# Kernel optimization log

Measured on AMD Instinct MI355X. Metric: run time of the kernel, lower is better.

The kernel has to match this reference:

```python
import jax, jax.numpy as jnp
import numpy as np

ALPHA = 1.0
B, N = 4096, 512


def _tv1d_row(y, lam):
    """Condat's direct 1-D TV denoising (exact port of the C reference used by prox_tv1d)."""
    n = y.shape[0]
    dt = y.dtype
    lam = jnp.asarray(lam, dt)
    idx = jnp.arange(n)

    def cond(s):
        return ~s[9]

    def body(s):
        k, k0, km, kp, vmin, vmax, umin, umax, x, done = s
        at_end = k == n - 1
        ynext = y[jnp.minimum(k + 1, n - 1)]
        # negative / positive jump tests (end-phase uses umin/umax sign tests)
        neg = jnp.where(at_end, umin < 0.0, ynext + umin < vmin - lam)
        pos = (~neg) & jnp.where(at_end, umax > 0.0, ynext + umax > vmax + lam)
        mid = (~neg) & (~pos)
        fin = mid & at_end
        mneg = neg & (~at_end)
        mpos = pos & (~at_end)
        mmid = mid & (~at_end)
        eneg = neg & at_end
        epos = pos & at_end
        # flush a finished segment of the output
        cnt_fin = (k - k0 + 1).astype(dt)
        hi = jnp.where(neg, km, jnp.where(pos, kp, n - 1))
        val = jnp.where(pos, vmax, jnp.where(fin, vmin + umin / cnt_fin, vmin))
        do_w = neg | pos | fin
        x = jnp.where(do_w & (idx >= k0) & (idx <= hi), val, x)
        nk = jnp.where(neg, km + 1, jnp.where(pos, kp + 1, k + 1))
        nk = jnp.minimum(nk, n - 1)
        ynk = y[nk]
        # plain accumulation step
        umin_t = umin + ynk - vmin
        umax_t = umax + ynk - vmax
        cnt = (nk - k0 + 1).astype(dt)
        c1 = umin_t >= lam
        c2 = umax_t <= -lam
        vmin_mid = jnp.where(c1, vmin + (umin_t - lam) / cnt, vmin)
        umin_mid = jnp.where(c1, lam, umin_t)
        km_mid = jnp.where(c1, nk, km)
        vmax_mid = jnp.where(c2, vmax + (umax_t + lam) / cnt, vmax)
        umax_mid = jnp.where(c2, -lam, umax_t)
        kp_mid = jnp.where(c2, nk, kp)
        jump = neg | pos
        nk0 = jnp.where(jump, nk, k0)
        nkm = jnp.where(neg | mpos, nk, jnp.where(mmid, km_mid, km))
        nkp = jnp.where(pos | mneg, nk, jnp.where(mmid, kp_mid, kp))
        nvmin = jnp.where(neg, ynk, jnp.where(mpos, ynk - 2.0 * lam, jnp.where(mmid, vmin_mid, vmin)))
        nvmax = jnp.where(pos, ynk, jnp.where(mneg, ynk + 2.0 * lam, jnp.where(mmid, vmax_mid, vmax)))
        numin = jnp.where(neg | mpos, lam, jnp.where(epos, ynk - lam - vmin, jnp.where(mmid, umin_mid, umin)))
        numax = jnp.where(pos | mneg, -lam, jnp.where(eneg, ynk + lam - vmax, jnp.where(mmid, umax_mid, umax)))
        nkk = jnp.where(fin, k, nk)
        return (nkk, nk0, nkm, nkp, nvmin, nvmax, numin, numax, x, done | fin)

    z = jnp.int32(0)
    s0 = (z, z, z, z, y[0] - lam, y[0] + lam, lam, -lam, jnp.zeros_like(y), jnp.array(False))
    return jax.lax.while_loop(cond, body, s0)[8]


def tv_prox(x, lam):
    return jax.vmap(lambda r: _tv1d_row(r, lam))(x)


def sparsemax(z):
    n = z.shape[-1]
    zs = -jnp.sort(-z, axis=-1)          # descending sort
    zc = jnp.cumsum(zs, axis=-1)
    r = jnp.arange(1, n + 1, dtype=z.dtype)
    supp = zs * r > (zc - 1.0)
    k = jnp.sum(supp, axis=-1, keepdims=True)
    tau = (jnp.take_along_axis(zc, k - 1, axis=-1) - 1.0) / k.astype(z.dtype)
    d = z - tau
    return jnp.where(d > 0.0, d, 0.0)


def setup_inputs():
    key = jax.random.key(0)
    x = jax.random.normal(key, (B, N), dtype=jnp.float32)
    return {"x": x}


def reference(x):
    # fusedmax(x) = sparsemax(prox_TV(x, alpha)), row-wise
    return sparsemax(tv_prox(x, ALPHA))
```

## Files before the change

kernel.cpp:

```cpp
#include <hip/hip_runtime.h>


#define TVN 512
#define LAMBDA 1.0f

__device__ __forceinline__ float wave_reduce_sum(float v) {
#pragma unroll
    for (int off = 32; off > 0; off >>= 1) v += __shfl_xor(v, off, 64);
    return v;
}

__global__ __launch_bounds__(64) void fusedmax_kernel(const float* __restrict__ xin,
                                                      float* __restrict__ out) {
    __shared__ alignas(16) float row[TVN + 8];
    const int t = threadIdx.x;
    const long long r = blockIdx.x;
    const float lam = LAMBDA;

    const float4* __restrict__ g4 = (const float4*)(xin + r * TVN);
    float4* s4 = (float4*)row;
    s4[t] = g4[t];
    s4[t + 64] = g4[t + 64];
    if (t < 8) row[TVN + t] = 0.0f;
    __syncthreads();

    if (t == 0) {
        const float yLast = row[TVN - 1];
        const float twolam = 2.0f * lam;
        int k = 0, k0 = 0, km = 0, kp = 0;
        float vmin = row[0] - lam, vmax = row[0] + lam;
        float umin = lam, umax = -lam;
        float cntf = 1.0f;
        float yn;

#define ACCUM_STEP(W)                                                   \
        yn = (W);                                                       \
        if (yn + umin < vmin - lam) goto neg_jump;                      \
        if (yn + umax > vmax + lam) goto pos_jump;                      \
        ++k; cntf += 1.0f;                                              \
        umin += yn - vmin;                                              \
        umax += yn - vmax;                                              \
        if (umin >= lam) {                                              \
            vmin += (umin - lam) * __builtin_amdgcn_rcpf(cntf);         \
            umin = lam; km = k;                                         \
        }                                                               \
        if (umax <= -lam) {                                             \
            vmax += (umax + lam) * __builtin_amdgcn_rcpf(cntf);         \
            umax = -lam; kp = k;                                        \
        }                                                               \
        if (k == TVN - 1) goto end_phase;

    refill: {
            float w0 = row[k + 1], w1 = row[k + 2], w2 = row[k + 3], w3 = row[k + 4];
            float w4 = row[k + 5], w5 = row[k + 6], w6 = row[k + 7], w7 = row[k + 8];
            ACCUM_STEP(w0)
            ACCUM_STEP(w1)
            ACCUM_STEP(w2)
            ACCUM_STEP(w3)
            ACCUM_STEP(w4)
            ACCUM_STEP(w5)
            ACCUM_STEP(w6)
            ACCUM_STEP(w7)
            goto refill;
        }
#undef ACCUM_STEP

    neg_jump: {
            for (int i = k0; i <= km; ++i) row[i] = vmin;
            const int nk = km + 1;
            const float ynk = row[nk];
            k = k0 = km = kp = nk;
            vmin = ynk;
            vmax = ynk + twolam;
            umin = lam;
            umax = -lam;
            cntf = 1.0f;
            if (k == TVN - 1) goto end_phase;
            goto refill;
        }

    pos_jump: {
            for (int i = k0; i <= kp; ++i) row[i] = vmax;
            const int nk = kp + 1;
            const float ynk = row[nk];
            k = k0 = km = kp = nk;
            vmax = ynk;
            vmin = ynk - twolam;
            umin = lam;
            umax = -lam;
            cntf = 1.0f;
            if (k == TVN - 1) goto end_phase;
            goto refill;
        }

    end_phase: {
            if (umin < 0.0f) {
                for (int i = k0; i <= km; ++i) row[i] = vmin;
                int nk = km + 1;
                const float ynk = (nk > TVN - 1) ? yLast : row[nk];
                if (nk > TVN - 1) nk = TVN - 1;
                k = k0 = km = nk;
                vmin = ynk;
                umin = lam;
                umax = ynk + lam - vmax;
                cntf = 1.0f;
                if (k == TVN - 1) goto end_phase;
                goto refill;
            } else if (umax > 0.0f) {
                for (int i = k0; i <= kp; ++i) row[i] = vmax;
                int nk = kp + 1;
                const float ynk = (nk > TVN - 1) ? yLast : row[nk];
                if (nk > TVN - 1) nk = TVN - 1;
                k = k0 = kp = nk;
                vmax = ynk;
                umax = -lam;
                umin = ynk - lam - vmin;
                cntf = 1.0f;
                if (k == TVN - 1) goto end_phase;
                goto refill;
            } else {
                const float v = vmin + umin / (float)(k - k0 + 1);
                for (int i = k0; i < TVN; ++i) row[i] = v;
            }
        }
    }
    __syncthreads();

    float4 a = s4[t];
    float4 b = s4[t + 64];
    float v[8] = {a.x, a.y, a.z, a.w, b.x, b.y, b.z, b.w};

    float ls = v[0] + v[1] + v[2] + v[3] + v[4] + v[5] + v[6] + v[7];
    float S = wave_reduce_sum(ls);
    float tau = (S - 1.0f) * (1.0f / (float)TVN);
    int cprev = TVN;
#pragma unroll 1
    for (int it = 0; it < 64; ++it) {
        float s = 0.0f, c = 0.0f;
#pragma unroll
        for (int j = 0; j < 8; ++j) {
            if (v[j] > tau) { s += v[j]; c += 1.0f; }
        }
        s = wave_reduce_sum(s);
        c = wave_reduce_sum(c);
        tau = (s - 1.0f) / c;
        int ci = (int)c;
        if (ci == cprev) break;
        cprev = ci;
    }

    float4 oa, ob;
    oa.x = fmaxf(v[0] - tau, 0.0f);
    oa.y = fmaxf(v[1] - tau, 0.0f);
    oa.z = fmaxf(v[2] - tau, 0.0f);
    oa.w = fmaxf(v[3] - tau, 0.0f);
    ob.x = fmaxf(v[4] - tau, 0.0f);
    ob.y = fmaxf(v[5] - tau, 0.0f);
    ob.z = fmaxf(v[6] - tau, 0.0f);
    ob.w = fmaxf(v[7] - tau, 0.0f);
    float4* __restrict__ o4 = (float4*)(out + r * TVN);
    o4[t] = oa;
    o4[t + 64] = ob;
}

extern "C" void kernel_launch(void* const* d_in, const int* in_sizes, int n_in,
                              void* d_out, int out_size, void* d_ws, size_t ws_size,
                              hipStream_t stream) {
    const float* x = (const float*)d_in[0];
    float* out = (float*)d_out;
    const int rows = in_sizes[0] / TVN;
    fusedmax_kernel<<<dim3(rows), dim3(64), 0, stream>>>(x, out);
}
```

Before: 262.5 us.

## Run TV denoising scan from both ends in parallel waves

Splits the serial Condat TV scan across two waves. One wave scans the row forward and the other scans a reversed copy, and each stops once a finalized segment reaches past the midpoint. The two halves are then stitched together for the sparsemax step, which roughly halves the serial dependency chain per row. The cost is a second shared buffer, a reversed staging copy, and redundant work when a segment straddles the midpoint. Correctness depends on finalized segments being exact in both scan directions.

```diff
diff --git a/kernel.cpp b/kernel.cpp
--- a/kernel.cpp
+++ b/kernel.cpp
@@ -3,6 +3,7 @@
 
 #define TVN 512
 #define LAMBDA 1.0f
+#define STOPK 257
 
 __device__ __forceinline__ float wave_reduce_sum(float v) {
 #pragma unroll
@@ -10,125 +11,153 @@
     return v;
 }
 
-__global__ __launch_bounds__(64) void fusedmax_kernel(const float* __restrict__ xin,
-                                                      float* __restrict__ out) {
-    __shared__ alignas(16) float row[TVN + 8];
-    const int t = threadIdx.x;
-    const long long r = blockIdx.x;
+__device__ __forceinline__ void tv_scan_half(float* __restrict__ row) {
     const float lam = LAMBDA;
-
-    const float4* __restrict__ g4 = (const float4*)(xin + r * TVN);
-    float4* s4 = (float4*)row;
-    s4[t] = g4[t];
-    s4[t + 64] = g4[t + 64];
-    if (t < 8) row[TVN + t] = 0.0f;
-    __syncthreads();
-
-    if (t == 0) {
-        const float yLast = row[TVN - 1];
-        const float twolam = 2.0f * lam;
-        int k = 0, k0 = 0, km = 0, kp = 0;
-        float vmin = row[0] - lam, vmax = row[0] + lam;
-        float umin = lam, umax = -lam;
-        float cntf = 1.0f;
-        float yn;
+    const float yLast = row[TVN - 1];
+    const float twolam = 2.0f * lam;
+    int k = 0, k0 = 0, km = 0, kp = 0;
+    float vmin = row[0] - lam, vmax = row[0] + lam;
+    float umin = lam, umax = -lam;
+    float cntf = 1.0f;
+    float yn;
 
 #define ACCUM_STEP(W)                                                   \
-        yn = (W);                                                       \
-        if (yn + umin < vmin - lam) goto neg_jump;                      \
-        if (yn + umax > vmax + lam) goto pos_jump;                      \
-        ++k; cntf += 1.0f;                                              \
-        umin += yn - vmin;                                              \
-        umax += yn - vmax;                                              \
-        if (umin >= lam) {                                              \
-            vmin += (umin - lam) * __builtin_amdgcn_rcpf(cntf);         \
-            umin = lam; km = k;                                         \
-        }                                                               \
-        if (umax <= -lam) {                                             \
-            vmax += (umax + lam) * __builtin_amdgcn_rcpf(cntf);         \
-            umax = -lam; kp = k;                                        \
-        }                                                               \
+    yn = (W);                                                           \
+    if (yn + umin < vmin - lam) goto neg_jump;                          \
+    if (yn + umax > vmax + lam) goto pos_jump;                          \
+    ++k; cntf += 1.0f;                                                  \
+    umin += yn - vmin;                                                  \
+    umax += yn - vmax;                                                  \
+    if (umin >= lam) {                                                  \
+        vmin += (umin - lam) * __builtin_amdgcn_rcpf(cntf);             \
+        umin = lam; km = k;                                             \
+    }                                                                   \
+    if (umax <= -lam) {                                                 \
+        vmax += (umax + lam) * __builtin_amdgcn_rcpf(cntf);             \
+        umax = -lam; kp = k;                                            \
+    }                                                                   \
+    if (k == TVN - 1) goto end_phase;
+
+refill: {
+        float w0 = row[k + 1], w1 = row[k + 2], w2 = row[k + 3], w3 = row[k + 4];
+        float w4 = row[k + 5], w5 = row[k + 6], w6 = row[k + 7], w7 = row[k + 8];
+        ACCUM_STEP(w0)
+        ACCUM_STEP(w1)
+        ACCUM_STEP(w2)
+        ACCUM_STEP(w3)
+        ACCUM_STEP(w4)
+        ACCUM_STEP(w5)
+        ACCUM_STEP(w6)
+        ACCUM_STEP(w7)
+        goto refill;
+    }
+#undef ACCUM_STEP
+
+neg_jump: {
+        for (int i = k0; i <= km; ++i) row[i] = vmin;
+        int nk = km + 1;
+        if (nk >= STOPK) return;
+        float ynk = row[nk];
+        k = k0 = km = kp = nk;
+        vmin = ynk;
+        vmax = ynk + twolam;
+        umin = lam;
+        umax = -lam;
+        cntf = 1.0f;
         if (k == TVN - 1) goto end_phase;
-
-    refill: {
-            float w0 = row[k + 1], w1 = row[k + 2], w2 = row[k + 3], w3 = row[k + 4];
-            float w4 = row[k + 5], w5 = row[k + 6], w6 = row[k + 7], w7 = row[k + 8];
-            ACCUM_STEP(w0)
-            ACCUM_STEP(w1)
-            ACCUM_STEP(w2)
-            ACCUM_STEP(w3)
-            ACCUM_STEP(w4)
-            ACCUM_STEP(w5)
-            ACCUM_STEP(w6)
-            ACCUM_STEP(w7)
-            goto refill;
-        }
-#undef ACCUM_STEP
-
-    neg_jump: {
-            for (int i = k0; i <= km; ++i) row[i] = vmin;
-            const int nk = km + 1;
-            const float ynk = row[nk];
-            k = k0 = km = kp = nk;
-            vmin = ynk;
-            vmax = ynk + twolam;
-            umin = lam;
-            umax = -lam;
-            cntf = 1.0f;
-            if (k == TVN - 1) goto end_phase;
-            goto refill;
-        }
-
-    pos_jump: {
-            for (int i = k0; i <= kp; ++i) row[i] = vmax;
-            const int nk = kp + 1;
-            const float ynk = row[nk];
-            k = k0 = km = kp = nk;
-            vmax = ynk;
-            vmin = ynk - twolam;
-            umin = lam;
-            umax = -lam;
-            cntf = 1.0f;
-            if (k == TVN - 1) goto end_phase;
-            goto refill;
-        }
-
-    end_phase: {
+        goto refill;
+    }
+
+pos_jump: {
+        for (int i = k0; i <= kp; ++i) row[i] = vmax;
+        int nk = kp + 1;
+        if (nk >= STOPK) return;
+        float ynk = row[nk];
+        k = k0 = km = kp = nk;
+        vmax = ynk;
+        vmin = ynk - twolam;
+        umin = lam;
+        umax = -lam;
+        cntf = 1.0f;
+        if (k == TVN - 1) goto end_phase;
+        goto refill;
+    }
+
+end_phase: {
+        for (;;) {
             if (umin < 0.0f) {
                 for (int i = k0; i <= km; ++i) row[i] = vmin;
                 int nk = km + 1;
-                const float ynk = (nk > TVN - 1) ? yLast : row[nk];
+                float ynk = (nk > TVN - 1) ? yLast : row[nk];
                 if (nk > TVN - 1) nk = TVN - 1;
                 k = k0 = km = nk;
                 vmin = ynk;
                 umin = lam;
                 umax = ynk + lam - vmax;
                 cntf = 1.0f;
-                if (k == TVN - 1) goto end_phase;
+                if (k == TVN - 1) continue;
                 goto refill;
             } else if (umax > 0.0f) {
                 for (int i = k0; i <= kp; ++i) row[i] = vmax;
                 int nk = kp + 1;
-                const float ynk = (nk > TVN - 1) ? yLast : row[nk];
+                float ynk = (nk > TVN - 1) ? yLast : row[nk];
                 if (nk > TVN - 1) nk = TVN - 1;
                 k = k0 = kp = nk;
                 vmax = ynk;
                 umax = -lam;
                 umin = ynk - lam - vmin;
                 cntf = 1.0f;
-                if (k == TVN - 1) goto end_phase;
+                if (k == TVN - 1) continue;
                 goto refill;
             } else {
-                const float v = vmin + umin / (float)(k - k0 + 1);
+                float v = vmin + umin / (float)(k - k0 + 1);
                 for (int i = k0; i < TVN; ++i) row[i] = v;
+                return;
             }
         }
     }
+}
+
+__global__ __launch_bounds__(128) void fusedmax_kernel(const float* __restrict__ xin,
+                                                       float* __restrict__ out) {
+    __shared__ alignas(16) float rowF[TVN + 8];
+    __shared__ alignas(16) float rowR[TVN + 8];
+
+    const int t = threadIdx.x;
+    const int w = t >> 6;
+    const int lane = t & 63;
+    const long long r = blockIdx.x;
+
+    const float4* __restrict__ g4 = (const float4*)(xin + r * TVN);
+    if (w == 0) {
+        float4* s4 = (float4*)rowF;
+        s4[lane] = g4[lane];
+        s4[lane + 64] = g4[lane + 64];
+        if (lane < 8) rowF[TVN + lane] = 0.0f;
+    } else {
+        float4 a = g4[lane];
+        float4 b = g4[lane + 64];
+        const int ba = 511 - 4 * lane;
+        rowR[ba] = a.x; rowR[ba - 1] = a.y; rowR[ba - 2] = a.z; rowR[ba - 3] = a.w;
+        const int bb = 255 - 4 * lane;
+        rowR[bb] = b.x; rowR[bb - 1] = b.y; rowR[bb - 2] = b.z; rowR[bb - 3] = b.w;
+        if (lane < 8) rowR[TVN + lane] = 0.0f;
+    }
     __syncthreads();
 
-    float4 a = s4[t];
-    float4 b = s4[t + 64];
-    float v[8] = {a.x, a.y, a.z, a.w, b.x, b.y, b.z, b.w};
+    if (lane == 0) tv_scan_half(w ? rowR : rowF);
+    __syncthreads();
+
+    float v[8];
+#pragma unroll
+    for (int j = 0; j < 4; ++j) v[j] = rowF[4 * lane + j];
+    {
+        const int i0 = 256 + 4 * lane;
+        v[4] = (i0 == 256) ? rowF[256] : rowR[511 - i0];
+        v[5] = rowR[511 - (i0 + 1)];
+        v[6] = rowR[511 - (i0 + 2)];
+        v[7] = rowR[511 - (i0 + 3)];
+    }
 
     float ls = v[0] + v[1] + v[2] + v[3] + v[4] + v[5] + v[6] + v[7];
     float S = wave_reduce_sum(ls);
@@ -149,18 +178,20 @@
         cprev = ci;
     }
 
-    float4 oa, ob;
-    oa.x = fmaxf(v[0] - tau, 0.0f);
-    oa.y = fmaxf(v[1] - tau, 0.0f);
-    oa.z = fmaxf(v[2] - tau, 0.0f);
-    oa.w = fmaxf(v[3] - tau, 0.0f);
-    ob.x = fmaxf(v[4] - tau, 0.0f);
-    ob.y = fmaxf(v[5] - tau, 0.0f);
-    ob.z = fmaxf(v[6] - tau, 0.0f);
-    ob.w = fmaxf(v[7] - tau, 0.0f);
+    float4 o;
+    if (w == 0) {
+        o.x = fmaxf(v[0] - tau, 0.0f);
+        o.y = fmaxf(v[1] - tau, 0.0f);
+        o.z = fmaxf(v[2] - tau, 0.0f);
+        o.w = fmaxf(v[3] - tau, 0.0f);
+    } else {
+        o.x = fmaxf(v[4] - tau, 0.0f);
+        o.y = fmaxf(v[5] - tau, 0.0f);
+        o.z = fmaxf(v[6] - tau, 0.0f);
+        o.w = fmaxf(v[7] - tau, 0.0f);
+    }
     float4* __restrict__ o4 = (float4*)(out + r * TVN);
-    o4[t] = oa;
-    o4[t + 64] = ob;
+    o4[lane + ((w == 0) ? 0 : 64)] = o;
 }
 
 extern "C" void kernel_launch(void* const* d_in, const int* in_sizes, int n_in,
@@ -169,5 +200,5 @@
     const float* x = (const float*)d_in[0];
     float* out = (float*)d_out;
     const int rows = in_sizes[0] / TVN;
-    fusedmax_kernel<<<dim3(rows), dim3(64), 0, stream>>>(x, out);
-}
+    fusedmax_kernel<<<dim3(rows), dim3(128), 0, stream>>>(x, out);
+}
```

After: 263.3 us. Within noise of the previous version (+0.3%).
